# Kernel optimization log

Measured on AMD Instinct MI355X. Metric: run time of the kernel, lower is better.

Reference implementation:

```python
import jax, jax.numpy as jnp
import numpy as np

B, D, E, H, TOP_K = 8192, 1024, 16, 1024, 8
LOSS_COEF = 0.01
NOISE_EPS = 0.01
INV_SQRT2 = 0.7071067811865476


def _normal_cdf(z):
    return 0.5 * (1.0 + jax.lax.erf(z * INV_SQRT2))


def _cv_squared(v):
    v = v.astype(jnp.float32)
    return jnp.var(v, ddof=1) / (jnp.mean(v) ** 2 + 1e-10)


def setup_inputs() -> dict:
    key = jax.random.key(0)
    k1, k2, k3, k4, k5, k6 = jax.random.split(key, 6)
    return {
        "x": jax.random.normal(k1, (B, D), dtype=jnp.float32),
        "w_gate": jax.random.normal(k2, (D, E), dtype=jnp.float32) * 0.02,
        "w_noise": jax.random.normal(k3, (D, E), dtype=jnp.float32) * 0.02,
        "expert_w": jax.random.normal(k4, (E, D, H), dtype=jnp.float32) * (1.0 / np.sqrt(D)),
        "expert_b": jax.random.normal(k5, (E, H), dtype=jnp.float32) * 0.01,
        "noise": jax.random.normal(k6, (B, E), dtype=jnp.float32),
    }


def reference(x, w_gate, w_noise, expert_w, expert_b, noise):
    # ---- noisy top-k gating (training=True) ----
    clean_logits = x @ w_gate                                   # [B, E]
    raw_noise_stddev = x @ w_noise                              # [B, E]
    noise_stddev = jax.nn.softplus(raw_noise_stddev) + NOISE_EPS
    noisy_logits = clean_logits + noise * noise_stddev          # [B, E]
    probs = jax.nn.softmax(noisy_logits, axis=1)                # [B, E]

    m = min(TOP_K + 1, E)
    top_logits, top_indices = jax.lax.top_k(probs, m)           # [B, m]
    top_k_logits = top_logits[:, :TOP_K]
    top_k_indices = top_indices[:, :TOP_K]
    top_k_gates = top_k_logits / (jnp.sum(top_k_logits, axis=1, keepdims=True) + 1e-6)

    rows = jnp.arange(B)[:, None]
    gates = jnp.zeros_like(probs).at[rows, top_k_indices].set(top_k_gates)  # [B, E]

    # ---- prob-in-top-k load (top_k < num_experts, training) ----
    # faithful to source: thresholds come from softmaxed top values,
    # compared against pre-softmax noisy/clean logits (as in original code)
    threshold_if_in = top_logits[:, TOP_K][:, None]             # [B, 1]
    threshold_if_out = top_logits[:, TOP_K - 1][:, None]        # [B, 1]
    is_in = noisy_logits > threshold_if_in
    prob_if_in = _normal_cdf((clean_logits - threshold_if_in) / noise_stddev)
    prob_if_out = _normal_cdf((clean_logits - threshold_if_out) / noise_stddev)
    load = jnp.where(is_in, prob_if_in, prob_if_out).sum(axis=0)  # [E]

    importance = gates.sum(axis=0)                              # [E]
    loss = LOSS_COEF * (_cv_squared(importance) + _cv_squared(load))

    # ---- experts: per-expert linear, gate-weighted sum over experts ----
    # y[b,h] = sum_e gates[b,e] * (x[b,:] @ W[e] + b[e])[h]
    y = jnp.einsum('bd,edh,be->bh', x, expert_w, gates) + gates @ expert_b
    return y, loss
```

## Files before the change

kernel.cpp:

```cpp
#include <hip/hip_runtime.h>
#include <cstdint>

#define B_SZ 8192
#define D_SZ 1024
#define E_SZ 16
#define H_SZ 1024
#define MAXTILES 544

using short8 = __attribute__((ext_vector_type(8))) short;
using f32x4  = __attribute__((ext_vector_type(4))) float;

__device__ __forceinline__ unsigned short f2bf(float f) {
  union { float f; unsigned int u; } v; v.f = f;
  unsigned int u = v.u;
  return (unsigned short)((u + 0x7fffu + ((u >> 16) & 1u)) >> 16);
}
__device__ __forceinline__ float bf2f(unsigned short h) {
  union { unsigned int u; float f; } v; v.u = ((unsigned int)h) << 16; return v.f;
}

__device__ __forceinline__ void async_ld16(void* lds, const void* g) {
  __builtin_amdgcn_global_load_lds(
      reinterpret_cast<const unsigned int __attribute__((address_space(1)))*>(
          reinterpret_cast<uintptr_t>(g)),
      reinterpret_cast<unsigned int __attribute__((address_space(3)))*>(
          reinterpret_cast<uintptr_t>(lds)),
      16, 0, 0);
}

__global__ __launch_bounds__(256) void prep(
    const float* __restrict__ x, const float* __restrict__ wg,
    const float* __restrict__ wn, const float* __restrict__ ew,
    unsigned short* __restrict__ xb, unsigned short* __restrict__ wtb,
    float* __restrict__ cl, float* __restrict__ rn, float* __restrict__ stats) {
  __shared__ __align__(16) float psm[2 * 32 * 132];
  const int bx = blockIdx.x;
  const int tid = threadIdx.x;

  if (bx < 256) {
    float* sx  = psm;
    float* swT = psm + 32 * 132;
    const int lane = tid & 63;
    const int wave = tid >> 6;
    const int row  = lane & 31;
    const int half = lane >> 5;
    const int rowbase = bx * 32;
    float acc[8] = {0.f, 0.f, 0.f, 0.f, 0.f, 0.f, 0.f, 0.f};

    const int srow = tid >> 3;
    const int sd   = (tid & 7) * 16;
    const int wd   = tid >> 1;
    const int wc   = (tid & 1) * 16;
    const float* wsrc = (wc == 0) ? wg : wn;

    for (int ch = 0; ch < 8; ++ch) {
      __syncthreads();
      #pragma unroll
      for (int k = 0; k < 4; ++k) {
        const float4 v = *(const float4*)(
            x + (size_t)(rowbase + srow) * D_SZ + ch * 128 + sd + k * 4);
        *(float4*)&sx[srow * 132 + sd + k * 4] = v;
      }
      {
        const float* wp = wsrc + (size_t)(ch * 128 + wd) * 16;
        float wv[16];
        #pragma unroll
        for (int k = 0; k < 4; ++k)
          *(float4*)&wv[k * 4] = *(const float4*)(wp + k * 4);
        #pragma unroll
        for (int j = 0; j < 16; ++j) swT[(wc + j) * 132 + wd] = wv[j];
      }
      __syncthreads();
      #pragma unroll 4
      for (int dg = 0; dg < 16; ++dg) {
        const int d = half * 64 + dg * 4;
        const f32x4 xv = *(const f32x4*)&sx[row * 132 + d];
        #pragma unroll
        for (int c = 0; c < 8; ++c) {
          const f32x4 wv = *(const f32x4*)&swT[(wave * 8 + c) * 132 + d];
          acc[c] = fmaf(xv[0], wv[0], acc[c]);
          acc[c] = fmaf(xv[1], wv[1], acc[c]);
          acc[c] = fmaf(xv[2], wv[2], acc[c]);
          acc[c] = fmaf(xv[3], wv[3], acc[c]);
        }
      }
    }
    #pragma unroll
    for (int c = 0; c < 8; ++c) acc[c] += __shfl_down(acc[c], 32);
    if (lane < 32) {
      const int cg = wave * 8;
      float* dst = (cg < 16) ? (cl + (size_t)(rowbase + row) * 16 + cg)
                             : (rn + (size_t)(rowbase + row) * 16 + (cg - 16));
      *(float4*)dst = *(const float4*)&acc[0];
      *(float4*)(dst + 4) = *(const float4*)&acc[4];
    }
  } else if (bx < 4352) {
    const int b = bx - 256;
    const size_t i = (size_t)b * 256 + tid;
    const float4 v0 = ((const float4*)x)[2 * i];
    const float4 v1 = ((const float4*)x)[2 * i + 1];
    unsigned short r[8] = {f2bf(v0.x), f2bf(v0.y), f2bf(v0.z), f2bf(v0.w),
                           f2bf(v1.x), f2bf(v1.y), f2bf(v1.z), f2bf(v1.w)};
    ((short8*)xb)[i] = *(const short8*)r;
    if (b == 0 && tid < 48) stats[tid] = 0.0f;
  } else {
    float (*t)[65] = (float(*)[65])psm;
    const int b = bx - 4352;
    const int e  = b >> 8;
    const int d0 = ((b >> 4) & 15) * 64;
    const int h0 = (b & 15) * 64;
    const float* We = ew + (size_t)e * D_SZ * H_SZ;
    unsigned short* Wte = wtb + (size_t)e * D_SZ * H_SZ;
    #pragma unroll
    for (int i = 0; i < 4; ++i) {
      const int idx = i * 256 + tid;
      const int r = idx >> 4, co = (idx & 15) * 4;
      *(float4*)&t[r][co] =
          *(const float4*)(We + (size_t)(d0 + r) * H_SZ + h0 + co);
    }
    __syncthreads();
    #pragma unroll
    for (int i = 0; i < 2; ++i) {
      const int idx = i * 256 + tid;
      const int r = idx >> 3, c8 = (idx & 7) * 8;
      unsigned short v[8];
      #pragma unroll
      for (int j = 0; j < 8; ++j) v[j] = f2bf(t[c8 + j][r]);
      *(short8*)(Wte + (size_t)(h0 + r) * D_SZ + d0 + c8) = *(const short8*)v;
    }
  }
}

__global__ __launch_bounds__(64) void gating_post(
    const float* __restrict__ clg, const float* __restrict__ rng,
    const float* __restrict__ noise, float* __restrict__ gates,
    float* __restrict__ stats, int* __restrict__ rowidx, int* __restrict__ rowmap) {
  int* gcount = (int*)(stats + 32);
  __shared__ int lcnt[16];
  __shared__ int lbase[16];
  const int row = blockIdx.x * 64 + threadIdx.x;
  if (threadIdx.x < 16) lcnt[threadIdx.x] = 0;
  float cl[16], sd[16], nl[16], p[16];
  #pragma unroll
  for (int e = 0; e < 16; ++e) {
    cl[e] = clg[(size_t)row * 16 + e];
    const float r = rng[(size_t)row * 16 + e];
    sd[e] = fmaxf(r, 0.0f) + log1pf(expf(-fabsf(r))) + 0.01f;
    nl[e] = cl[e] + noise[(size_t)row * 16 + e] * sd[e];
  }
  float mx = nl[0];
  #pragma unroll
  for (int e = 1; e < 16; ++e) mx = fmaxf(mx, nl[e]);
  float sum = 0.0f;
  #pragma unroll
  for (int e = 0; e < 16; ++e) { p[e] = expf(nl[e] - mx); sum += p[e]; }
  const float inv = 1.0f / sum;
  #pragma unroll
  for (int e = 0; e < 16; ++e) p[e] *= inv;
  float tmp[16];
  #pragma unroll
  for (int e = 0; e < 16; ++e) tmp[e] = p[e];
  float tv[9]; int ti[9];
  for (int k = 0; k < 9; ++k) {
    float bv = tmp[0]; int bj = 0;
    #pragma unroll
    for (int j = 1; j < 16; ++j) if (tmp[j] > bv) { bv = tmp[j]; bj = j; }
    tv[k] = bv; ti[k] = bj; tmp[bj] = -1.0f;
  }
  float s8 = 0.0f;
  #pragma unroll
  for (int k = 0; k < 8; ++k) s8 += tv[k];
  const float denom = s8 + 1e-6f;
  float g[16];
  #pragma unroll
  for (int e = 0; e < 16; ++e) g[e] = 0.0f;
  for (int k = 0; k < 8; ++k) g[ti[k]] = tv[k] / denom;
  const float thr_in = tv[8], thr_out = tv[7];
  float lc[16];
  #pragma unroll
  for (int e = 0; e < 16; ++e) {
    const float t = (nl[e] > thr_in) ? thr_in : thr_out;
    lc[e] = 0.5f * (1.0f + erff(((cl[e] - t) / sd[e]) * 0.70710678118654752f));
  }
  #pragma unroll
  for (int e = 0; e < 16; ++e) gates[(size_t)row * 16 + e] = g[e];
  __syncthreads();
  int myslot[8];
  #pragma unroll
  for (int k = 0; k < 8; ++k) myslot[k] = atomicAdd(&lcnt[ti[k]], 1);
  __syncthreads();
  if (threadIdx.x < 16) lbase[threadIdx.x] = atomicAdd(&gcount[threadIdx.x], lcnt[threadIdx.x]);
  __syncthreads();
  #pragma unroll
  for (int k = 0; k < 8; ++k) {
    const int e = ti[k];
    const int slot = lbase[e] + myslot[k];
    rowidx[e * B_SZ + slot] = row;
    rowmap[row * 8 + k] = (e << 13) | slot;
  }
  #pragma unroll
  for (int e = 0; e < 16; ++e) {
    float vi = g[e], vl = lc[e];
    for (int o = 32; o > 0; o >>= 1) { vi += __shfl_down(vi, o); vl += __shfl_down(vl, o); }
    if (threadIdx.x == 0) {
      atomicAdd(&stats[e], vi);
      atomicAdd(&stats[16 + e], vl);
    }
  }
}

__global__ __launch_bounds__(256, 4) void moe_gemm(
    const unsigned short* __restrict__ Xb,
    const unsigned short* __restrict__ Wt,
    const float* __restrict__ gates,
    const float* __restrict__ ebias,
    const float* __restrict__ stats,
    const int* __restrict__ rowidx,
    unsigned short* __restrict__ partial) {
  __shared__ __align__(16) char smem[34816 + 512 + 512];
  unsigned short* sA = (unsigned short*)smem;
  unsigned short* sB = (unsigned short*)(smem + 16384);
  unsigned short* sOut = (unsigned short*)smem;
  float* sGG = (float*)(smem + 34816);
  int*   sRI = (int*)(smem + 34816 + 512);

  const int* gcount = (const int*)(stats + 32);
  int my_e = -1, tile = 0, tstart = 0, acc_t = 0;
  #pragma unroll
  for (int ee = 0; ee < 16; ++ee) {
    const int nt_e = (gcount[ee] + 127) >> 7;
    if (my_e < 0 && (int)blockIdx.y < acc_t + nt_e) {
      my_e = ee; tile = blockIdx.y - acc_t; tstart = acc_t;
    }
    acc_t += nt_e;
  }
  if (my_e < 0) return;
  const int e = my_e;
  const int slot0 = tile << 7;
  const int cnt = gcount[e];
  const int col0 = blockIdx.x << 7;
  const int pb = tstart << 7;

  const int tid  = threadIdx.x;
  const int lane = tid & 63;
  const int wave = tid >> 6;
  const int wm = wave >> 1, wn = wave & 1;
  const int ml = lane & 15;
  const int quad = lane >> 4;
  const int wbase = tid & ~63;

  if (tid < 128) {
    const int slot = slot0 + tid;
    const int ok = slot < cnt;
    const int row = ok ? rowidx[e * B_SZ + slot] : 0;
    sRI[tid] = row;
    sGG[tid] = ok ? gates[(size_t)row * 16 + e] : 0.0f;
  }
  float ebv[4];
  #pragma unroll
  for (int j = 0; j < 4; ++j)
    ebv[j] = ebias[(size_t)e * H_SZ + col0 + wn * 64 + j * 16 + ml];
  __syncthreads();

  const unsigned short* We = Wt + (size_t)e * D_SZ * H_SZ;
  const unsigned short* aptr[4];
  const unsigned short* bptr[4];
  #pragma unroll
  for (int i = 0; i < 4; ++i) {
    const int s = i * 256 + tid;
    const int m = s >> 3, pp = s & 7;
    const int gc = pp ^ (m & 7);
    aptr[i] = Xb + (size_t)sRI[m] * D_SZ + gc * 8;
    bptr[i] = We + (size_t)(col0 + m) * D_SZ + gc * 8;
  }

  f32x4 acc[4][4] = {};
  for (int kb = 0; kb < 16; ++kb) {
    const int k0 = kb * 64;
    __syncthreads();
    #pragma unroll
    for (int i = 0; i < 4; ++i)
      async_ld16(sA + (size_t)(i * 256 + wbase) * 8, aptr[i] + k0);
    #pragma unroll
    for (int i = 0; i < 4; ++i)
      async_ld16(sB + (size_t)(i * 256 + wbase) * 8, bptr[i] + k0);
    __syncthreads();
    #pragma unroll
    for (int kk = 0; kk < 2; ++kk) {
      short8 af[4], bfr[4];
      #pragma unroll
      for (int i = 0; i < 4; ++i) {
        const int m = wm * 64 + i * 16 + ml;
        const int cA = kk * 4 + quad;
        af[i]  = *(const short8*)(sA + ((size_t)m * 8 + (cA ^ (m & 7))) * 8);
        const int n = wn * 64 + i * 16 + ml;
        bfr[i] = *(const short8*)(sB + ((size_t)n * 8 + (cA ^ (n & 7))) * 8);
      }
      #pragma unroll
      for (int i = 0; i < 4; ++i)
        #pragma unroll
        for (int j = 0; j < 4; ++j)
          acc[i][j] = __builtin_amdgcn_mfma_f32_16x16x32_bf16(af[i], bfr[j], acc[i][j], 0, 0, 0);
    }
  }

  __syncthreads();
  #pragma unroll
  for (int i = 0; i < 4; ++i) {
    const int mbase = wm * 64 + i * 16 + quad * 4;
    #pragma unroll
    for (int r = 0; r < 4; ++r) {
      const int mrow = mbase + r;
      const float gv = sGG[mrow];
      #pragma unroll
      for (int j = 0; j < 4; ++j) {
        const int cc = wn * 64 + j * 16 + ml;
        sOut[mrow * 136 + cc] = f2bf(gv * (acc[i][j][r] + ebv[j]));
      }
    }
  }
  __syncthreads();
  const size_t prow0 = (size_t)(pb + slot0);
  #pragma unroll
  for (int it = 0; it < 8; ++it) {
    const int s = it * 256 + tid;
    const int rr = s >> 4;
    const int c8 = (s & 15) * 8;
    const short8 v = *(const short8*)(sOut + rr * 136 + c8);
    __builtin_nontemporal_store(
        v, (short8*)(partial + (prow0 + rr) * H_SZ + col0 + c8));
  }
}

__global__ __launch_bounds__(256) void reduce_k(
    const unsigned short* __restrict__ partial, const int* __restrict__ rowmap,
    const float* __restrict__ stats, float* __restrict__ y) {
  const int row0 = blockIdx.x * 4;
  const int tid = threadIdx.x;
  const int* gcount = (const int*)(stats + 32);
  __shared__ int sp[4][8];
  if (tid < 32) {
    const int r = tid >> 3, k = tid & 7;
    const int v = rowmap[(row0 + r) * 8 + k];
    const int e = v >> 13, slot = v & 8191;
    int t = 0;
    #pragma unroll
    for (int ee = 0; ee < 16; ++ee) t += (ee < e) ? ((gcount[ee] + 127) >> 7) : 0;
    sp[r][k] = (t << 7) + slot;
  }
  __syncthreads();
  const int r = tid >> 6;
  const int c0 = (tid & 63) * 16;
  float a[16];
  #pragma unroll
  for (int j = 0; j < 16; ++j) a[j] = 0.f;
  #pragma unroll
  for (int k = 0; k < 8; ++k) {
    const unsigned short* pp = partial + (size_t)sp[r][k] * H_SZ + c0;
    const short8 p0 = *(const short8*)pp;
    const short8 p1 = *(const short8*)(pp + 8);
    #pragma unroll
    for (int j = 0; j < 8; ++j) {
      a[j]     += bf2f((unsigned short)p0[j]);
      a[j + 8] += bf2f((unsigned short)p1[j]);
    }
  }
  float* yp = y + (size_t)(row0 + r) * H_SZ + c0;
  #pragma unroll
  for (int q = 0; q < 4; ++q) {
    float4 o = {a[q * 4], a[q * 4 + 1], a[q * 4 + 2], a[q * 4 + 3]};
    *(float4*)(yp + q * 4) = o;
  }

  if (blockIdx.x == 0 && tid == 0) {
    double si = 0.0, sl = 0.0;
    for (int e = 0; e < 16; ++e) { si += stats[e]; sl += stats[16 + e]; }
    const double mi = si / 16.0, mld = sl / 16.0;
    double vi = 0.0, vl = 0.0;
    for (int e = 0; e < 16; ++e) {
      const double di = stats[e] - mi;       vi += di * di;
      const double dl = stats[16 + e] - mld; vl += dl * dl;
    }
    vi /= 15.0; vl /= 15.0;
    const double loss = 0.01 * (vi / (mi * mi + 1e-10) + vl / (mld * mld + 1e-10));
    y[(size_t)B_SZ * H_SZ] = (float)loss;
  }
}

extern "C" void kernel_launch(void* const* d_in, const int* in_sizes, int n_in,
                              void* d_out, int out_size, void* d_ws, size_t ws_size,
                              hipStream_t stream) {
  (void)in_sizes; (void)n_in; (void)out_size; (void)ws_size;
  const float* x    = (const float*)d_in[0];
  const float* wg   = (const float*)d_in[1];
  const float* wnoi = (const float*)d_in[2];
  const float* ew   = (const float*)d_in[3];
  const float* eb   = (const float*)d_in[4];
  const float* nz   = (const float*)d_in[5];
  float* y = (float*)d_out;

  char* ws = (char*)d_ws;
  const size_t MB = 1024 * 1024;
  unsigned short* xb     = (unsigned short*)(ws);
  unsigned short* wtb    = (unsigned short*)(ws + 16 * MB);
  float* cl              = (float*)(ws + 48 * MB);
  float* rn              = (float*)(ws + 48 * MB + 512 * 1024);
  float* gates           = (float*)(ws + 49 * MB);
  int*   rowidx          = (int*)  (ws + 49 * MB + 512 * 1024);
  int*   rowmap          = (int*)  (ws + 50 * MB);
  float* stats           = (float*)(ws + 50 * MB + 512 * 1024);
  unsigned short* partial= (unsigned short*)(ws + 52 * MB);

  hipLaunchKernelGGL(prep,        dim3(8448),        dim3(256), 0, stream,
                     x, wg, wnoi, ew, xb, wtb, cl, rn, stats);
  hipLaunchKernelGGL(gating_post, dim3(128),         dim3(64),  0, stream,
                     cl, rn, nz, gates, stats, rowidx, rowmap);
  hipLaunchKernelGGL(moe_gemm,    dim3(8, MAXTILES), dim3(256), 0, stream,
                     xb, wtb, gates, eb, stats, rowidx, partial);
  hipLaunchKernelGGL(reduce_k,    dim3(2048),        dim3(256), 0, stream,
                     partial, rowmap, stats, y);
}
```

Baseline: 409.0 us.

## Enlarge MoE GEMM tiles to 256x256 with double-buffered async LDS pipeline

The grouped expert GEMM now uses 256x256 output tiles, 512-thread blocks (8 waves, each computing 128x64) and 128KB of LDS. A/B tiles are double-buffered, and the loads for the next k-steps are interleaved between MFMA groups under s_setprio. Explicit vmcnt waits and barriers replace the full syncthreads loop. The aim is more reuse of each loaded tile and global loads hidden behind MFMA work, at the cost of more padding per expert (256-row granularity), fewer blocks, and higher register and LDS pressure that limits occupancy.

```diff
diff --git a/kernel.cpp b/kernel.cpp
--- a/kernel.cpp
+++ b/kernel.cpp
@@ -5,7 +5,7 @@
 #define D_SZ 1024
 #define E_SZ 16
 #define H_SZ 1024
-#define MAXTILES 544
+#define MAXTILES 272
 
 using short8 = __attribute__((ext_vector_type(8))) short;
 using f32x4  = __attribute__((ext_vector_type(4))) float;
@@ -209,7 +209,7 @@
   }
 }
 
-__global__ __launch_bounds__(256, 4) void moe_gemm(
+__global__ __launch_bounds__(512, 2) void moe_gemm(
     const unsigned short* __restrict__ Xb,
     const unsigned short* __restrict__ Wt,
     const float* __restrict__ gates,
@@ -217,118 +217,159 @@
     const float* __restrict__ stats,
     const int* __restrict__ rowidx,
     unsigned short* __restrict__ partial) {
-  __shared__ __align__(16) char smem[34816 + 512 + 512];
-  unsigned short* sA = (unsigned short*)smem;
-  unsigned short* sB = (unsigned short*)(smem + 16384);
-  unsigned short* sOut = (unsigned short*)smem;
-  float* sGG = (float*)(smem + 34816);
-  int*   sRI = (int*)(smem + 34816 + 512);
+  __shared__ __align__(16) char smem[133120];
+  int*   sRI = (int*)(smem + 131072);
+  float* sGG = (float*)(smem + 132096);
 
   const int* gcount = (const int*)(stats + 32);
   int my_e = -1, tile = 0, tstart = 0, acc_t = 0;
   #pragma unroll
   for (int ee = 0; ee < 16; ++ee) {
-    const int nt_e = (gcount[ee] + 127) >> 7;
+    const int nt_e = (gcount[ee] + 255) >> 8;
     if (my_e < 0 && (int)blockIdx.y < acc_t + nt_e) {
-      my_e = ee; tile = blockIdx.y - acc_t; tstart = acc_t;
+      my_e = ee; tile = (int)blockIdx.y - acc_t; tstart = acc_t;
     }
     acc_t += nt_e;
   }
   if (my_e < 0) return;
   const int e = my_e;
-  const int slot0 = tile << 7;
+  const int slot0 = tile << 8;
   const int cnt = gcount[e];
-  const int col0 = blockIdx.x << 7;
-  const int pb = tstart << 7;
-
-  const int tid  = threadIdx.x;
+  const int col0 = (int)blockIdx.x << 8;
+
+  const int tid  = (int)threadIdx.x;
   const int lane = tid & 63;
   const int wave = tid >> 6;
-  const int wm = wave >> 1, wn = wave & 1;
+  const int wm = wave >> 2, wn = wave & 3;
   const int ml = lane & 15;
   const int quad = lane >> 4;
-  const int wbase = tid & ~63;
-
-  if (tid < 128) {
+  const int wb = tid & ~63;
+
+  if (tid < 256) {
     const int slot = slot0 + tid;
     const int ok = slot < cnt;
     const int row = ok ? rowidx[e * B_SZ + slot] : 0;
     sRI[tid] = row;
     sGG[tid] = ok ? gates[(size_t)row * 16 + e] : 0.0f;
   }
+  __syncthreads();
+
+  const int gc = (tid & 7) ^ ((tid >> 3) & 7);
+  const int rl = tid >> 3;
+  const unsigned short* const We = Wt + (size_t)e * D_SZ * H_SZ;
+  const unsigned short* a_src0 = Xb + (size_t)sRI[rl]       * D_SZ + gc * 8;
+  const unsigned short* a_src1 = Xb + (size_t)sRI[64 + rl]  * D_SZ + gc * 8;
+  const unsigned short* a_src2 = Xb + (size_t)sRI[128 + rl] * D_SZ + gc * 8;
+  const unsigned short* a_src3 = Xb + (size_t)sRI[192 + rl] * D_SZ + gc * 8;
+  const unsigned short* b_src0 = We + (size_t)(col0 + rl)   * D_SZ + gc * 8;
+
+#define STG_A(kt, l) \
+  async_ld16(smem + (((kt) & 1) * 32768) + ((((l) * 512 + wb)) << 4), \
+             a_src##l + (kt) * 64)
+#define STG_B(kt, l) \
+  async_ld16(smem + 65536 + (((kt) & 1) * 32768) + ((((l) * 512 + wb)) << 4), \
+             b_src0 + (l) * 65536 + (kt) * 64)
+
+  STG_A(0,0); STG_A(0,1);  STG_A(0,2); STG_A(0,3);
+  STG_B(0,0); STG_B(0,1);  STG_B(0,2); STG_B(0,3);
+  STG_A(1,0); STG_A(1,1);  STG_A(1,2); STG_A(1,3);
+  STG_B(1,0); STG_B(1,1);
+  asm volatile("s_waitcnt vmcnt(6)" ::: "memory");
+  __builtin_amdgcn_s_barrier();
+
+  f32x4 acc[8][4] = {};
+
+#define MF16(I0) \
+  do { __builtin_amdgcn_s_setprio(1); \
+    _Pragma("unroll") for (int ii = 0; ii < 2; ++ii) \
+      _Pragma("unroll") for (int j = 0; j < 4; ++j) \
+        _Pragma("unroll") for (int kk = 0; kk < 2; ++kk) \
+          acc[(I0)+ii][j] = __builtin_amdgcn_mfma_f32_16x16x32_bf16( \
+              af[(I0)+ii][kk], bf[j][kk], acc[(I0)+ii][j], 0, 0, 0); \
+    __builtin_amdgcn_s_setprio(0); } while (0)
+
+  #pragma unroll
+  for (int kt = 0; kt < 16; ++kt) {
+    const unsigned short* sAb =
+        (const unsigned short*)(smem + ((kt & 1) ? 32768 : 0));
+    const unsigned short* sBb =
+        (const unsigned short*)(smem + 65536 + ((kt & 1) ? 32768 : 0));
+    if (kt + 1 < 16) { STG_B(kt+1,2); STG_B(kt+1,3); }
+    short8 af[8][2], bf[4][2];
+    #pragma unroll
+    for (int i = 0; i < 8; ++i) {
+      const int m = wm * 128 + i * 16 + ml;
+      #pragma unroll
+      for (int kk = 0; kk < 2; ++kk) {
+        const int c = (kk * 4 + quad) ^ (m & 7);
+        af[i][kk] = *(const short8*)(sAb + (size_t)(m * 8 + c) * 8);
+      }
+    }
+    #pragma unroll
+    for (int j = 0; j < 4; ++j) {
+      const int n = wn * 64 + j * 16 + ml;
+      #pragma unroll
+      for (int kk = 0; kk < 2; ++kk) {
+        const int c = (kk * 4 + quad) ^ (n & 7);
+        bf[j][kk] = *(const short8*)(sBb + (size_t)(n * 8 + c) * 8);
+      }
+    }
+    MF16(0);
+    asm volatile("s_waitcnt lgkmcnt(0)" ::: "memory");
+    __builtin_amdgcn_s_barrier();
+    if (kt + 2 < 16) { STG_A(kt+2,0); STG_A(kt+2,1); }
+    MF16(2);
+    if (kt + 2 < 16) { STG_A(kt+2,2); STG_A(kt+2,3); }
+    MF16(4);
+    if (kt + 2 < 16) { STG_B(kt+2,0); STG_B(kt+2,1); }
+    MF16(6);
+    if (kt <= 13) {
+      asm volatile("s_waitcnt vmcnt(6)" ::: "memory");
+      __builtin_amdgcn_s_barrier();
+    } else if (kt == 14) {
+      asm volatile("s_waitcnt vmcnt(0)" ::: "memory");
+      __builtin_amdgcn_s_barrier();
+    }
+  }
+#undef MF16
+#undef STG_A
+#undef STG_B
+
+  __syncthreads();
   float ebv[4];
   #pragma unroll
   for (int j = 0; j < 4; ++j)
     ebv[j] = ebias[(size_t)e * H_SZ + col0 + wn * 64 + j * 16 + ml];
-  __syncthreads();
-
-  const unsigned short* We = Wt + (size_t)e * D_SZ * H_SZ;
-  const unsigned short* aptr[4];
-  const unsigned short* bptr[4];
-  #pragma unroll
-  for (int i = 0; i < 4; ++i) {
-    const int s = i * 256 + tid;
-    const int m = s >> 3, pp = s & 7;
-    const int gc = pp ^ (m & 7);
-    aptr[i] = Xb + (size_t)sRI[m] * D_SZ + gc * 8;
-    bptr[i] = We + (size_t)(col0 + m) * D_SZ + gc * 8;
-  }
-
-  f32x4 acc[4][4] = {};
-  for (int kb = 0; kb < 16; ++kb) {
-    const int k0 = kb * 64;
+  unsigned short* sOut = (unsigned short*)smem;
+  const size_t prow0 = (size_t)((tstart << 8) + slot0);
+  #pragma unroll
+  for (int half = 0; half < 2; ++half) {
+    if (wm == half) {
+      #pragma unroll
+      for (int i = 0; i < 8; ++i) {
+        const int lr = i * 16 + quad * 4;
+        #pragma unroll
+        for (int r = 0; r < 4; ++r) {
+          const float gv = sGG[half * 128 + lr + r];
+          #pragma unroll
+          for (int j = 0; j < 4; ++j) {
+            const int cc = wn * 64 + j * 16 + ml;
+            sOut[(lr + r) * 264 + cc] = f2bf(gv * (acc[i][j][r] + ebv[j]));
+          }
+        }
+      }
+    }
     __syncthreads();
     #pragma unroll
-    for (int i = 0; i < 4; ++i)
-      async_ld16(sA + (size_t)(i * 256 + wbase) * 8, aptr[i] + k0);
-    #pragma unroll
-    for (int i = 0; i < 4; ++i)
-      async_ld16(sB + (size_t)(i * 256 + wbase) * 8, bptr[i] + k0);
+    for (int it = 0; it < 8; ++it) {
+      const int s = it * 512 + tid;
+      const int rr = s >> 5;
+      const int c8 = (s & 31) * 8;
+      const short8 v = *(const short8*)(sOut + rr * 264 + c8);
+      __builtin_nontemporal_store(
+          v, (short8*)(partial + (prow0 + half * 128 + rr) * H_SZ + col0 + c8));
+    }
     __syncthreads();
-    #pragma unroll
-    for (int kk = 0; kk < 2; ++kk) {
-      short8 af[4], bfr[4];
-      #pragma unroll
-      for (int i = 0; i < 4; ++i) {
-        const int m = wm * 64 + i * 16 + ml;
-        const int cA = kk * 4 + quad;
-        af[i]  = *(const short8*)(sA + ((size_t)m * 8 + (cA ^ (m & 7))) * 8);
-        const int n = wn * 64 + i * 16 + ml;
-        bfr[i] = *(const short8*)(sB + ((size_t)n * 8 + (cA ^ (n & 7))) * 8);
-      }
-      #pragma unroll
-      for (int i = 0; i < 4; ++i)
-        #pragma unroll
-        for (int j = 0; j < 4; ++j)
-          acc[i][j] = __builtin_amdgcn_mfma_f32_16x16x32_bf16(af[i], bfr[j], acc[i][j], 0, 0, 0);
-    }
-  }
-
-  __syncthreads();
-  #pragma unroll
-  for (int i = 0; i < 4; ++i) {
-    const int mbase = wm * 64 + i * 16 + quad * 4;
-    #pragma unroll
-    for (int r = 0; r < 4; ++r) {
-      const int mrow = mbase + r;
-      const float gv = sGG[mrow];
-      #pragma unroll
-      for (int j = 0; j < 4; ++j) {
-        const int cc = wn * 64 + j * 16 + ml;
-        sOut[mrow * 136 + cc] = f2bf(gv * (acc[i][j][r] + ebv[j]));
-      }
-    }
-  }
-  __syncthreads();
-  const size_t prow0 = (size_t)(pb + slot0);
-  #pragma unroll
-  for (int it = 0; it < 8; ++it) {
-    const int s = it * 256 + tid;
-    const int rr = s >> 4;
-    const int c8 = (s & 15) * 8;
-    const short8 v = *(const short8*)(sOut + rr * 136 + c8);
-    __builtin_nontemporal_store(
-        v, (short8*)(partial + (prow0 + rr) * H_SZ + col0 + c8));
   }
 }
 
@@ -345,8 +386,8 @@
     const int e = v >> 13, slot = v & 8191;
     int t = 0;
     #pragma unroll
-    for (int ee = 0; ee < 16; ++ee) t += (ee < e) ? ((gcount[ee] + 127) >> 7) : 0;
-    sp[r][k] = (t << 7) + slot;
+    for (int ee = 0; ee < 16; ++ee) t += (ee < e) ? ((gcount[ee] + 255) >> 8) : 0;
+    sp[r][k] = (t << 8) + slot;
   }
   __syncthreads();
   const int r = tid >> 6;
@@ -411,12 +452,12 @@
   float* stats           = (float*)(ws + 50 * MB + 512 * 1024);
   unsigned short* partial= (unsigned short*)(ws + 52 * MB);
 
-  hipLaunchKernelGGL(prep,        dim3(8448),        dim3(256), 0, stream,
+  hipLaunchKernelGGL(prep,        dim3(8448),         dim3(256), 0, stream,
                      x, wg, wnoi, ew, xb, wtb, cl, rn, stats);
-  hipLaunchKernelGGL(gating_post, dim3(128),         dim3(64),  0, stream,
+  hipLaunchKernelGGL(gating_post, dim3(128),          dim3(64),  0, stream,
                      cl, rn, nz, gates, stats, rowidx, rowmap);
-  hipLaunchKernelGGL(moe_gemm,    dim3(8, MAXTILES), dim3(256), 0, stream,
+  hipLaunchKernelGGL(moe_gemm,    dim3(4, MAXTILES),  dim3(512), 0, stream,
                      xb, wtb, gates, eb, stats, rowidx, partial);
-  hipLaunchKernelGGL(reduce_k,    dim3(2048),        dim3(256), 0, stream,
+  hipLaunchKernelGGL(reduce_k,    dim3(2048),         dim3(256), 0, stream,
                      partial, rowmap, stats, y);
 }
```

Result: faster. 391.3 us (-4.3%).

## Restructure MoE GEMM to 128x256 tiles with double-buffered k-loop and XCD swizzle

Applied to the files above, without the earlier changes.

The grouped expert GEMM now uses 512-thread blocks, each computing a 128x256 output tile with 8 waves. Its k-loop is double-buffered with K=32 stages, so the async load of the next stage overlaps the MFMAs of the current one, and each iteration needs one barrier instead of two. MFMA sections are raised in priority with s_setprio. A 1D grid with a blockIdx remap keeps neighbouring tiles on the same XCD for L2 reuse. The epilogue is split into two halves to fit shared memory, which adds barriers, and the larger LDS footprint may reduce occupancy.

```diff
diff --git a/kernel.cpp b/kernel.cpp
--- a/kernel.cpp
+++ b/kernel.cpp
@@ -209,7 +209,7 @@
   }
 }
 
-__global__ __launch_bounds__(256, 4) void moe_gemm(
+__global__ __launch_bounds__(512, 4) void moe_gemm(
     const unsigned short* __restrict__ Xb,
     const unsigned short* __restrict__ Wt,
     const float* __restrict__ gates,
@@ -217,20 +217,22 @@
     const float* __restrict__ stats,
     const int* __restrict__ rowidx,
     unsigned short* __restrict__ partial) {
-  __shared__ __align__(16) char smem[34816 + 512 + 512];
-  unsigned short* sA = (unsigned short*)smem;
-  unsigned short* sB = (unsigned short*)(smem + 16384);
-  unsigned short* sOut = (unsigned short*)smem;
-  float* sGG = (float*)(smem + 34816);
-  int*   sRI = (int*)(smem + 34816 + 512);
+  __shared__ __align__(16) char smem[49152 + 512 + 512];
+  int*   sRI = (int*)(smem + 49152);
+  float* sGG = (float*)(smem + 49664);
+
+  const int orig = (int)blockIdx.x;
+  const int logical = (orig & 7) * 272 + (orig >> 3);
+  const int tileY = logical >> 2;
+  const int col  = logical & 3;
 
   const int* gcount = (const int*)(stats + 32);
   int my_e = -1, tile = 0, tstart = 0, acc_t = 0;
   #pragma unroll
   for (int ee = 0; ee < 16; ++ee) {
     const int nt_e = (gcount[ee] + 127) >> 7;
-    if (my_e < 0 && (int)blockIdx.y < acc_t + nt_e) {
-      my_e = ee; tile = blockIdx.y - acc_t; tstart = acc_t;
+    if (my_e < 0 && tileY < acc_t + nt_e) {
+      my_e = ee; tile = tileY - acc_t; tstart = acc_t;
     }
     acc_t += nt_e;
   }
@@ -238,16 +240,15 @@
   const int e = my_e;
   const int slot0 = tile << 7;
   const int cnt = gcount[e];
-  const int col0 = blockIdx.x << 7;
-  const int pb = tstart << 7;
-
-  const int tid  = threadIdx.x;
+  const int col0 = col << 8;
+
+  const int tid  = (int)threadIdx.x;
   const int lane = tid & 63;
   const int wave = tid >> 6;
-  const int wm = wave >> 1, wn = wave & 1;
+  const int wm = wave >> 2, wn = wave & 3;
   const int ml = lane & 15;
   const int quad = lane >> 4;
-  const int wbase = tid & ~63;
+  const int wb = tid & ~63;
 
   if (tid < 128) {
     const int slot = slot0 + tid;
@@ -256,79 +257,91 @@
     sRI[tid] = row;
     sGG[tid] = ok ? gates[(size_t)row * 16 + e] : 0.0f;
   }
+  __syncthreads();
+
+  const int sr = tid >> 2;
+  const int sc = (tid & 3) ^ (sr & 3);
+  const unsigned short* const We = Wt + (size_t)e * D_SZ * H_SZ;
+  const unsigned short* a_srcp = Xb + (size_t)sRI[sr] * D_SZ + sc * 8;
+  const unsigned short* b_src0 = We + (size_t)(col0 + sr) * D_SZ + sc * 8;
+  const unsigned short* b_src1 = b_src0 + 128 * D_SZ;
+
+#define STG(kt) do {                                                        \
+    const int o_ = ((kt) & 1);                                              \
+    async_ld16(smem + o_ * 8192 + (wb << 4), a_srcp + (kt) * 32);           \
+    async_ld16(smem + 16384 + o_ * 16384 + (wb << 4), b_src0 + (kt) * 32);  \
+    async_ld16(smem + 16384 + o_ * 16384 + 8192 + (wb << 4),                \
+               b_src1 + (kt) * 32);                                         \
+  } while (0)
+
+  STG(0);
+  __syncthreads();
+
+  f32x4 acc[4][4] = {};
   float ebv[4];
   #pragma unroll
   for (int j = 0; j < 4; ++j)
     ebv[j] = ebias[(size_t)e * H_SZ + col0 + wn * 64 + j * 16 + ml];
-  __syncthreads();
-
-  const unsigned short* We = Wt + (size_t)e * D_SZ * H_SZ;
-  const unsigned short* aptr[4];
-  const unsigned short* bptr[4];
-  #pragma unroll
-  for (int i = 0; i < 4; ++i) {
-    const int s = i * 256 + tid;
-    const int m = s >> 3, pp = s & 7;
-    const int gc = pp ^ (m & 7);
-    aptr[i] = Xb + (size_t)sRI[m] * D_SZ + gc * 8;
-    bptr[i] = We + (size_t)(col0 + m) * D_SZ + gc * 8;
-  }
-
-  f32x4 acc[4][4] = {};
-  for (int kb = 0; kb < 16; ++kb) {
-    const int k0 = kb * 64;
+
+  #pragma unroll 2
+  for (int kt = 0; kt < 32; ++kt) {
+    if (kt + 1 < 32) STG(kt + 1);
+    const unsigned short* sA = (const unsigned short*)(smem + (kt & 1) * 8192);
+    const unsigned short* sB =
+        (const unsigned short*)(smem + 16384 + (kt & 1) * 16384);
+    short8 af[4], bfr[4];
+    #pragma unroll
+    for (int i = 0; i < 4; ++i) {
+      const int m = wm * 64 + i * 16 + ml;
+      af[i] = *(const short8*)(sA + m * 32 + (quad ^ (m & 3)) * 8);
+    }
+    #pragma unroll
+    for (int j = 0; j < 4; ++j) {
+      const int n = wn * 64 + j * 16 + ml;
+      bfr[j] = *(const short8*)(sB + n * 32 + (quad ^ (n & 3)) * 8);
+    }
+    __builtin_amdgcn_s_setprio(1);
+    #pragma unroll
+    for (int i = 0; i < 4; ++i)
+      #pragma unroll
+      for (int j = 0; j < 4; ++j)
+        acc[i][j] = __builtin_amdgcn_mfma_f32_16x16x32_bf16(
+            af[i], bfr[j], acc[i][j], 0, 0, 0);
+    __builtin_amdgcn_s_setprio(0);
     __syncthreads();
-    #pragma unroll
-    for (int i = 0; i < 4; ++i)
-      async_ld16(sA + (size_t)(i * 256 + wbase) * 8, aptr[i] + k0);
-    #pragma unroll
-    for (int i = 0; i < 4; ++i)
-      async_ld16(sB + (size_t)(i * 256 + wbase) * 8, bptr[i] + k0);
-    __syncthreads();
-    #pragma unroll
-    for (int kk = 0; kk < 2; ++kk) {
-      short8 af[4], bfr[4];
+  }
+#undef STG
+
+  unsigned short* sOut = (unsigned short*)smem;
+  const size_t prow0 = (size_t)((tstart << 7) + slot0);
+  #pragma unroll
+  for (int h = 0; h < 2; ++h) {
+    if (wm == h) {
       #pragma unroll
       for (int i = 0; i < 4; ++i) {
-        const int m = wm * 64 + i * 16 + ml;
-        const int cA = kk * 4 + quad;
-        af[i]  = *(const short8*)(sA + ((size_t)m * 8 + (cA ^ (m & 7))) * 8);
-        const int n = wn * 64 + i * 16 + ml;
-        bfr[i] = *(const short8*)(sB + ((size_t)n * 8 + (cA ^ (n & 7))) * 8);
+        const int lr = i * 16 + quad * 4;
+        #pragma unroll
+        for (int r = 0; r < 4; ++r) {
+          const float gv = sGG[h * 64 + lr + r];
+          #pragma unroll
+          for (int j = 0; j < 4; ++j) {
+            const int cc = wn * 64 + j * 16 + ml;
+            sOut[(lr + r) * 264 + cc] = f2bf(gv * (acc[i][j][r] + ebv[j]));
+          }
+        }
       }
-      #pragma unroll
-      for (int i = 0; i < 4; ++i)
-        #pragma unroll
-        for (int j = 0; j < 4; ++j)
-          acc[i][j] = __builtin_amdgcn_mfma_f32_16x16x32_bf16(af[i], bfr[j], acc[i][j], 0, 0, 0);
-    }
-  }
-
-  __syncthreads();
-  #pragma unroll
-  for (int i = 0; i < 4; ++i) {
-    const int mbase = wm * 64 + i * 16 + quad * 4;
-    #pragma unroll
-    for (int r = 0; r < 4; ++r) {
-      const int mrow = mbase + r;
-      const float gv = sGG[mrow];
-      #pragma unroll
-      for (int j = 0; j < 4; ++j) {
-        const int cc = wn * 64 + j * 16 + ml;
-        sOut[mrow * 136 + cc] = f2bf(gv * (acc[i][j][r] + ebv[j]));
-      }
-    }
-  }
-  __syncthreads();
-  const size_t prow0 = (size_t)(pb + slot0);
-  #pragma unroll
-  for (int it = 0; it < 8; ++it) {
-    const int s = it * 256 + tid;
-    const int rr = s >> 4;
-    const int c8 = (s & 15) * 8;
-    const short8 v = *(const short8*)(sOut + rr * 136 + c8);
-    __builtin_nontemporal_store(
-        v, (short8*)(partial + (prow0 + rr) * H_SZ + col0 + c8));
+    }
+    __syncthreads();
+    #pragma unroll
+    for (int it = 0; it < 4; ++it) {
+      const int s = it * 512 + tid;
+      const int rr = s >> 5;
+      const int c8 = (s & 31) * 8;
+      const short8 v = *(const short8*)(sOut + rr * 264 + c8);
+      __builtin_nontemporal_store(
+          v, (short8*)(partial + (prow0 + h * 64 + rr) * H_SZ + col0 + c8));
+    }
+    __syncthreads();
   }
 }
 
@@ -411,12 +424,12 @@
   float* stats           = (float*)(ws + 50 * MB + 512 * 1024);
   unsigned short* partial= (unsigned short*)(ws + 52 * MB);
 
-  hipLaunchKernelGGL(prep,        dim3(8448),        dim3(256), 0, stream,
+  hipLaunchKernelGGL(prep,        dim3(8448),          dim3(256), 0, stream,
                      x, wg, wnoi, ew, xb, wtb, cl, rn, stats);
-  hipLaunchKernelGGL(gating_post, dim3(128),         dim3(64),  0, stream,
+  hipLaunchKernelGGL(gating_post, dim3(128),           dim3(64),  0, stream,
                      cl, rn, nz, gates, stats, rowidx, rowmap);
-  hipLaunchKernelGGL(moe_gemm,    dim3(8, MAXTILES), dim3(256), 0, stream,
+  hipLaunchKernelGGL(moe_gemm,    dim3(4 * MAXTILES),  dim3(512), 0, stream,
                      xb, wtb, gates, eb, stats, rowidx, partial);
-  hipLaunchKernelGGL(reduce_k,    dim3(2048),        dim3(256), 0, stream,
+  hipLaunchKernelGGL(reduce_k,    dim3(2048),          dim3(256), 0, stream,
                      partial, rowmap, stats, y);
 }
```

After: 392.7 us. 4.0% less time.
